# Kernel optimization log

Hardware: AMD Instinct MI355X
Metric: run time of the kernel (lower is better)

The kernel has to match this reference:

```python
import jax, jax.numpy as jnp
import numpy as np

B, S, D, H = 2, 2048, 1024, 16
DH = D // H  # 64

def setup_inputs() -> dict:
    key = jax.random.key(0)
    ks = jax.random.split(key, 11)
    sc = 1.0 / np.sqrt(D)
    return {
        "query": jax.random.normal(ks[0], (B, S, D), jnp.float32),
        "key":   jax.random.normal(ks[1], (B, S, D), jnp.float32),
        "value": jax.random.normal(ks[2], (B, S, D), jnp.float32),
        "Wq": jax.random.normal(ks[3], (D, D), jnp.float32) * sc,
        "bq": jnp.zeros((D,), jnp.float32),
        "Wk": jax.random.normal(ks[4], (D, D), jnp.float32) * sc,
        "bk": jnp.zeros((D,), jnp.float32),
        "Wv": jax.random.normal(ks[5], (D, D), jnp.float32) * sc,
        "bv": jnp.zeros((D,), jnp.float32),
        "Wo": jax.random.normal(ks[6], (D, D), jnp.float32) * sc,
        "bo": jnp.zeros((D,), jnp.float32),
    }

def reference(query, key, value, Wq, bq, Wk, bk, Wv, bv, Wo, bo):
    # torch Linear: y = x @ W^T + b
    def split_heads(x):  # (B,S,D) -> (B,H,S,DH)
        return x.reshape(B, S, H, DH).transpose(0, 2, 1, 3)
    Q = split_heads(query @ Wq.T + bq)
    K = split_heads(key   @ Wk.T + bk)
    V = split_heads(value @ Wv.T + bv)
    scores = jnp.einsum('bhqd,bhkd->bhqk', Q, K) / jnp.sqrt(jnp.float32(DH))
    # Original applies torch.softmax(scores, dim=1) on a (B*H, Sq, Sk) tensor,
    # i.e. normalization over the QUERY axis -> axis=-2 here (faithful to source).
    attn = jax.nn.softmax(scores, axis=-2)
    # dropout omitted for deterministic reference (identity / eval mode)
    out = jnp.einsum('bhqk,bhkd->bhqd', attn, V)  # (B,H,S,DH)
    out = out.transpose(0, 2, 1, 3).reshape(B, S, D)
    return out @ Wo.T + bo
```

## Files before the change

### kernel.cpp

```cpp
#include <hip/hip_runtime.h>
#include <hip/hip_bf16.h>
#include <math.h>

#define BB 2
#define SS 2048
#define DD 1024
#define HH 16
#define DH 64

typedef __bf16 bf16;
typedef __bf16 bf16x8 __attribute__((ext_vector_type(8)));
typedef __bf16 bf16x4 __attribute__((ext_vector_type(4)));
typedef short short4v __attribute__((ext_vector_type(4)));
typedef float f32x4 __attribute__((ext_vector_type(4)));

static const size_t NTOK  = (size_t)BB * SS * DD;


__device__ __forceinline__ f32x4 mfma16(bf16x8 a, bf16x8 b, f32x4 c) {
    return __builtin_amdgcn_mfma_f32_16x16x32_bf16(a, b, c, 0, 0, 0);
}
__device__ __forceinline__ f32x4 mfma16k16(short4v a, short4v b, f32x4 c) {
    return __builtin_amdgcn_mfma_f32_16x16x16bf16_1k(a, b, c, 0, 0, 0);
}
__device__ __forceinline__ void gload_lds16(const void* g, void* l) {
    __builtin_amdgcn_global_load_lds(
        (const __attribute__((address_space(1))) void*)g,
        (__attribute__((address_space(3))) void*)l, 16, 0, 0);
}
__device__ __forceinline__ bf16x8 cvt8(float4 a, float4 b) {
    bf16x8 r;
    r[0] = (bf16)a.x; r[1] = (bf16)a.y; r[2] = (bf16)a.z; r[3] = (bf16)a.w;
    r[4] = (bf16)b.x; r[5] = (bf16)b.y; r[6] = (bf16)b.z; r[7] = (bf16)b.w;
    return r;
}

#define WAITV(N)  asm volatile("s_waitcnt vmcnt(" #N ")" ::: "memory")
#define BAR()     __builtin_amdgcn_s_barrier()

__global__ void signal_f(float* out, float v) {
    if (threadIdx.x == 0 && blockIdx.x == 0) out[0] = v;
}

__global__ __launch_bounds__(256) void cvt_bf16(
    const float* __restrict__ s, bf16* __restrict__ d)
{
    size_t i = ((size_t)blockIdx.x * 256 + threadIdx.x) * 8;
    float4 a = *(const float4*)(s + i);
    float4 b = *(const float4*)(s + i + 4);
    *(bf16x8*)(d + i) = cvt8(a, b);
}
__global__ __launch_bounds__(256) void cvt_w3(
    const float* __restrict__ w0, const float* __restrict__ w1,
    const float* __restrict__ w2, bf16* __restrict__ o0,
    bf16* __restrict__ o1, bf16* __restrict__ o2)
{
    const float* s = (blockIdx.y == 0) ? w0 : (blockIdx.y == 1) ? w1 : w2;
    bf16*        d = (blockIdx.y == 0) ? o0 : (blockIdx.y == 1) ? o1 : o2;
    size_t i = ((size_t)blockIdx.x * 256 + threadIdx.x) * 8;
    float4 a = *(const float4*)(s + i);
    float4 b = *(const float4*)(s + i + 4);
    *(bf16x8*)(d + i) = cvt8(a, b);
}

#define LDP3 40

__global__ __launch_bounds__(256, 3) void qkv4(
    const float* __restrict__ Aq, const float* __restrict__ Ak,
    const float* __restrict__ Av,
    const bf16* __restrict__ Wqb, const bf16* __restrict__ Wkb,
    const bf16* __restrict__ Wvb,
    const float* __restrict__ bq, const float* __restrict__ bk,
    const float* __restrict__ bv,
    bf16* __restrict__ Qs, bf16* __restrict__ Ks, bf16* __restrict__ Vt)
{
    const int K = DD, N = DD;
    __shared__ bf16 As[2][128][LDP3];
    __shared__ bf16 Bs[2][128][LDP3];

    int t = (int)threadIdx.x;
    int lane = t & 63, w = t >> 6;
    int wm = w >> 1, wn = w & 1;
    int c16 = lane & 15, quad = lane >> 4, ko = quad << 3;

    int x = blockIdx.x & 7;
    int j = blockIdx.x >> 3;
    int proj = j >> 5;
    int rem  = j & 31;
    int tm = x + ((rem >> 3) << 3);
    int tn = rem & 7;

    const float* A    = (proj == 0) ? Aq : (proj == 1) ? Ak : Av;
    const bf16*  W    = (proj == 0) ? Wqb : (proj == 1) ? Wkb : Wvb;
    const float* bias = (proj == 0) ? bq : (proj == 1) ? bk : bv;
    bf16*        C    = (proj == 0) ? Qs : (proj == 1) ? Ks : Vt;
    float osc = (proj == 0) ? 0.125f : 1.0f;

    int arow = t >> 1, acb = (t & 1) * 16;
    const float* abase = A + (size_t)(tm * 128 + arow) * K + acb;
    const bf16*  wbase = W + (size_t)(tn * 128 + arow) * K + acb;

    f32x4 acc[4][4];
#pragma unroll
    for (int i = 0; i < 4; ++i)
#pragma unroll
        for (int q = 0; q < 4; ++q) acc[i][q] = (f32x4){0.f, 0.f, 0.f, 0.f};

    float4 av0, av1, av2, av3;
    bf16x8 wv0, wv1;
    av0 = *(const float4*)(abase);     av1 = *(const float4*)(abase + 4);
    av2 = *(const float4*)(abase + 8); av3 = *(const float4*)(abase + 12);
    wv0 = *(const bf16x8*)(wbase);
    wv1 = *(const bf16x8*)(wbase + 8);
    *(bf16x8*)&As[0][arow][acb]     = cvt8(av0, av1);
    *(bf16x8*)&As[0][arow][acb + 8] = cvt8(av2, av3);
    *(bf16x8*)&Bs[0][arow][acb]     = wv0;
    *(bf16x8*)&Bs[0][arow][acb + 8] = wv1;
    __syncthreads();

    int bi = 0;
    for (int k0 = 0; k0 < K; k0 += 32) {
        int kn = k0 + 32;
        if (kn < K) {
            av0 = *(const float4*)(abase + kn);
            av1 = *(const float4*)(abase + kn + 4);
            av2 = *(const float4*)(abase + kn + 8);
            av3 = *(const float4*)(abase + kn + 12);
            wv0 = *(const bf16x8*)(wbase + kn);
            wv1 = *(const bf16x8*)(wbase + kn + 8);
        }
        bf16x8 af[4], bfr[4];
#pragma unroll
        for (int mt = 0; mt < 4; ++mt)
            af[mt] = *(const bf16x8*)&As[bi][wm * 64 + mt * 16 + c16][ko];
#pragma unroll
        for (int nt = 0; nt < 4; ++nt)
            bfr[nt] = *(const bf16x8*)&Bs[bi][wn * 64 + nt * 16 + c16][ko];
#pragma unroll
        for (int mt = 0; mt < 4; ++mt)
#pragma unroll
            for (int nt = 0; nt < 4; ++nt)
                acc[mt][nt] = mfma16(af[mt], bfr[nt], acc[mt][nt]);

        if (kn < K) {
            *(bf16x8*)&As[bi ^ 1][arow][acb]     = cvt8(av0, av1);
            *(bf16x8*)&As[bi ^ 1][arow][acb + 8] = cvt8(av2, av3);
            *(bf16x8*)&Bs[bi ^ 1][arow][acb]     = wv0;
            *(bf16x8*)&Bs[bi ^ 1][arow][acb + 8] = wv1;
        }
        __syncthreads();
        bi ^= 1;
    }

#pragma unroll
    for (int nt = 0; nt < 4; ++nt) {
        int col = tn * 128 + wn * 64 + nt * 16 + c16;
        float bv2 = bias[col];
#pragma unroll
        for (int mt = 0; mt < 4; ++mt) {
            int r0 = tm * 128 + wm * 64 + mt * 16 + quad * 4;
            if (proj == 2) {
                int b2 = r0 >> 11;
                int s  = r0 & (SS - 1);
                size_t base = ((size_t)b2 * N + col) * SS + s;
                bf16x4 pk;
#pragma unroll
                for (int r = 0; r < 4; ++r)
                    pk[r] = (bf16)(acc[mt][nt][r] + bv2);
                *(bf16x4*)&C[base] = pk;
            } else {
#pragma unroll
                for (int r = 0; r < 4; ++r)
                    C[(size_t)(r0 + r) * N + col] =
                        (bf16)((acc[mt][nt][r] + bv2) * osc);
            }
        }
    }
}

__global__ __launch_bounds__(256) void gemm5(
    const bf16* __restrict__ A, const bf16* __restrict__ W,
    const float* __restrict__ bias, float* __restrict__ C)
{
    __shared__ __align__(16) bf16 As[4][128][32];
    __shared__ __align__(16) bf16 Bs[4][128][32];

    int t = (int)threadIdx.x;
    int lane = t & 63, w = t >> 6;
    int wm = w >> 1, wn = w & 1;
    int c16 = lane & 15, quad = lane >> 4, ko = quad << 3;

    int x = blockIdx.x & 7, j = blockIdx.x >> 3;
    int tm = x + ((j >> 3) << 3);
    int tn = j & 7;

    int wr0 = lane >> 2;
    int wsw = (lane & 3) ^ (wr0 & 3);
    const bf16* asrc = A + (size_t)(tm * 128 + w * 32 + wr0) * DD + wsw * 8;
    const bf16* wsrc = W + (size_t)(tn * 128 + w * 32 + wr0) * DD + wsw * 8;
    char* adst = (char*)&As[0][0][0] + w * 2048;
    char* wdst = (char*)&Bs[0][0][0] + w * 2048;

    f32x4 acc[4][4];
#pragma unroll
    for (int i = 0; i < 4; ++i)
#pragma unroll
        for (int q = 0; q < 4; ++q) acc[i][q] = (f32x4){0.f, 0.f, 0.f, 0.f};

#pragma unroll
    for (int s = 0; s < 2; ++s) {
        gload_lds16(asrc + s * 32, adst + s * 8192);
        gload_lds16(asrc + (size_t)16 * DD + s * 32, adst + s * 8192 + 1024);
        gload_lds16(wsrc + s * 32, wdst + s * 8192);
        gload_lds16(wsrc + (size_t)16 * DD + s * 32, wdst + s * 8192 + 1024);
    }

    for (int t0 = 0; t0 < 32; ++t0) {
        if (t0 + 2 < 32) {
            int s = t0 + 2, sb = (s & 3) * 8192;
            gload_lds16(asrc + s * 32, adst + sb);
            gload_lds16(asrc + (size_t)16 * DD + s * 32, adst + sb + 1024);
            gload_lds16(wsrc + s * 32, wdst + sb);
            gload_lds16(wsrc + (size_t)16 * DD + s * 32, wdst + sb + 1024);
        }
        if (t0 < 30)      { WAITV(8); }
        else if (t0 == 30){ WAITV(4); }
        else              { WAITV(0); }
        BAR();
        const char* al = (const char*)&As[0][0][0] + (t0 & 3) * 8192;
        const char* wl = (const char*)&Bs[0][0][0] + (t0 & 3) * 8192;
        bf16x8 af[4], bfr[4];
#pragma unroll
        for (int mt = 0; mt < 4; ++mt) {
            int row = wm * 64 + mt * 16 + c16;
            af[mt] = *(const bf16x8*)(al + row * 64 + ((quad ^ (row & 3)) << 4));
        }
#pragma unroll
        for (int nt = 0; nt < 4; ++nt) {
            int row = wn * 64 + nt * 16 + c16;
            bfr[nt] = *(const bf16x8*)(wl + row * 64 + ((quad ^ (row & 3)) << 4));
        }
#pragma unroll
        for (int mt = 0; mt < 4; ++mt)
#pragma unroll
            for (int nt = 0; nt < 4; ++nt)
                acc[mt][nt] = mfma16(af[mt], bfr[nt], acc[mt][nt]);
    }

#pragma unroll
    for (int nt = 0; nt < 4; ++nt) {
        int col = tn * 128 + wn * 64 + nt * 16 + c16;
        float bv = bias[col];
#pragma unroll
        for (int mt = 0; mt < 4; ++mt) {
            int r0 = tm * 128 + wm * 64 + mt * 16 + quad * 4;
#pragma unroll
            for (int r = 0; r < 4; ++r)
                C[(size_t)(r0 + r) * DD + col] = acc[mt][nt][r] + bv;
        }
    }
}

__global__ __launch_bounds__(512) void col_stats4(
    const bf16* __restrict__ Q, const bf16* __restrict__ Km,
    float* __restrict__ rzS)
{
    __shared__ __align__(16) bf16 Qlds[4][32][64];

    int t = (int)threadIdx.x;
    int w = t >> 6, lane = t & 63;
    int c16 = lane & 15, quad = lane >> 4, ko = quad << 3;

    int x = blockIdx.x & 7, j = blockIdx.x >> 3;
    int bh = ((j >> 3) << 3) + x;
    int kg = j & 7;
    int b = bh >> 4, h = bh & (HH - 1);
    int kbase = kg * 256 + w * 32;

    bf16x8 kf[2][2];
#pragma unroll
    for (int g = 0; g < 2; ++g) {
        const bf16* kp =
            Km + ((size_t)(b * SS + kbase + g * 16 + c16)) * DD + h * DH + ko;
        kf[g][0] = *(const bf16x8*)kp;
        kf[g][1] = *(const bf16x8*)(kp + 32);
    }

    int srow  = ((w & 3) << 3) + (lane >> 3);
    int schnk = (lane & 7) ^ (srow & 7);
    const bf16* gsrc = Q + ((size_t)(b * SS + srow)) * DD + h * DH + schnk * 8;
    int ldsOff = (w & 3) << 10;
    bool stager = (w < 4);

    float z[2][4] = {{0.f,0.f,0.f,0.f},{0.f,0.f,0.f,0.f}};

    if (stager) {
        gload_lds16(gsrc, (char*)&Qlds[0][0][0] + ldsOff);
        gload_lds16(gsrc + (size_t)32 * DD, (char*)&Qlds[1][0][0] + ldsOff);
    }

    for (int t0 = 0; t0 < 64; ++t0) {
        if (t0 + 2 < 64 && stager)
            gload_lds16(gsrc + (size_t)(t0 + 2) * 32 * DD,
                        (char*)&Qlds[(t0 + 2) & 3][0][0] + ldsOff);
        if (t0 < 62)      { WAITV(2); }
        else if (t0 == 62){ WAITV(1); }
        else              { WAITV(0); }
        BAR();
        const char* ql = (const char*)&Qlds[t0 & 3][0][0];
#pragma unroll
        for (int qs = 0; qs < 2; ++qs) {
            int row = qs * 16 + c16;
            int p0  = quad ^ (row & 7);
            bf16x8 qf0 = *(const bf16x8*)(ql + row * 128 + p0 * 16);
            bf16x8 qf1 = *(const bf16x8*)(ql + row * 128 + (p0 ^ 4) * 16);
#pragma unroll
            for (int g = 0; g < 2; ++g) {
                f32x4 a = {0.f, 0.f, 0.f, 0.f};
                a = mfma16(kf[g][0], qf0, a);
                a = mfma16(kf[g][1], qf1, a);
#pragma unroll
                for (int r = 0; r < 4; ++r)
                    z[g][r] += __expf(a[r]);
            }
        }
    }

#pragma unroll
    for (int g = 0; g < 2; ++g)
#pragma unroll
        for (int r = 0; r < 4; ++r) {
#pragma unroll
            for (int off = 1; off < 16; off <<= 1)
                z[g][r] += __shfl_xor(z[g][r], off, 64);
        }
    if (c16 == 0) {
        size_t base = (size_t)bh * SS + kbase + quad * 4;
#pragma unroll
        for (int g = 0; g < 2; ++g)
#pragma unroll
            for (int r = 0; r < 4; ++r)
                rzS[base + g * 16 + r] = 1.0f / z[g][r];
    }
}

__global__ __launch_bounds__(512) void attn_ctx6(
    const bf16* __restrict__ Q, const bf16* __restrict__ Km,
    const bf16* __restrict__ Vt, const float* __restrict__ rzS,
    bf16* __restrict__ ctx)
{
    __shared__ __align__(16) char lds[4][8192];

    int t = (int)threadIdx.x;
    int w = t >> 6, lane = t & 63;
    int c16 = lane & 15, quad = lane >> 4, ko = quad << 3;

    int bid = blockIdx.x;
    int x = bid & 7, j = bid >> 3;
    int bh = ((j >> 3) << 3) + x;
    int qg = j & 7;
    int b = bh >> 4, h = bh & (HH - 1);
    int qt0 = qg * 16 + w * 2;

    const bf16* qp0 = Q + ((size_t)(b * SS + qt0 * 16 + c16)) * DD + h * DH + ko;
    bf16x8 qa0 = *(const bf16x8*)qp0;
    bf16x8 qa1 = *(const bf16x8*)(qp0 + 32);
    const bf16* qp1 = qp0 + (size_t)16 * DD;
    bf16x8 qb0 = *(const bf16x8*)qp1;
    bf16x8 qb1 = *(const bf16x8*)(qp1 + 32);

    const bf16* gsrc;
    int ldsOff;
    bool isK = (w < 4);
    if (isK) {
        int row   = (w << 3) + (lane >> 3);
        int chunk = (lane & 7) ^ (row & 7);
        gsrc  = Km + ((size_t)(b * SS + row)) * DD + h * DH + chunk * 8;
        ldsOff = (w << 10);
    } else {
        int i = w - 4;
        int row   = (i << 4) + (lane >> 2);
        int chunk = (lane & 3) ^ (row & 3);
        gsrc  = Vt + ((size_t)(b * DD + h * DH + row)) * SS + chunk * 8;
        ldsOff = 4096 + (i << 10);
    }

    int kread  = c16 * 128 + ((quad ^ (c16 & 7)) << 4);
    int vread0 = c16 * 64 + (((quad >> 1) ^ (c16 & 3)) << 4) + ((quad & 1) << 3);

    const float* rzp = rzS + (size_t)bh * SS + quad * 4;

    f32x4 oa[4] = {{0,0,0,0},{0,0,0,0},{0,0,0,0},{0,0,0,0}};
    f32x4 ob[4] = {{0,0,0,0},{0,0,0,0},{0,0,0,0},{0,0,0,0}};

    gload_lds16(gsrc, &lds[0][ldsOff]);
    gload_lds16(isK ? gsrc + (size_t)32 * DD : gsrc + 32, &lds[1][ldsOff]);

    for (int t0 = 0; t0 < 64; ++t0) {
        if (t0 + 2 < 64) {
            int s = t0 + 2;
            const bf16* g = isK ? gsrc + (size_t)(s * 32) * DD : gsrc + s * 32;
            gload_lds16(g, &lds[s & 3][ldsOff]);
        }
        if (t0 < 62)      { WAITV(2); }
        else if (t0 == 62){ WAITV(1); }
        else              { WAITV(0); }
        BAR();
        const char* kl = &lds[t0 & 3][0];
        const char* vl = &lds[t0 & 3][4096];
        int kb = t0 * 32;
#pragma unroll
        for (int ks = 0; ks < 2; ++ks) {
            int kb0 = kread + ks * 2048;
            bf16x8 kf0 = *(const bf16x8*)(kl + kb0);
            bf16x8 kf1 = *(const bf16x8*)(kl + (kb0 ^ 64));
            f32x4 z4 = *(const f32x4*)(rzp + kb + ks * 16);
            f32x4 sa = {0,0,0,0}, sb = {0,0,0,0};
            sa = mfma16(kf0, qa0, sa);
            sa = mfma16(kf1, qa1, sa);
            sb = mfma16(kf0, qb0, sb);
            sb = mfma16(kf1, qb1, sb);

            union { bf16x4 b; short4v s; } pa, pb;
#pragma unroll
            for (int r = 0; r < 4; ++r) {
                pa.b[r] = (bf16)(__expf(sa[r]) * z4[r]);
                pb.b[r] = (bf16)(__expf(sb[r]) * z4[r]);
            }
            int vb0 = ks ? (vread0 ^ 32) : vread0;
#pragma unroll
            for (int dt = 0; dt < 4; ++dt) {
                short4v vf = *(const short4v*)(vl + vb0 + dt * 1024);
                oa[dt] = mfma16k16(pa.s, vf, oa[dt]);
                ob[dt] = mfma16k16(pb.s, vf, ob[dt]);
            }
        }
    }

    size_t orow = ((size_t)(b * SS + qt0 * 16 + quad * 4)) * DD + h * DH + c16;
#pragma unroll
    for (int dt = 0; dt < 4; ++dt)
#pragma unroll
        for (int r = 0; r < 4; ++r) {
            ctx[orow + (size_t)r * DD + dt * 16] = (bf16)oa[dt][r];
            ctx[orow + (size_t)(16 + r) * DD + dt * 16] = (bf16)ob[dt][r];
        }
}

extern "C" void kernel_launch(void* const* d_in, const int* in_sizes, int n_in,
                              void* d_out, int out_size, void* d_ws, size_t ws_size,
                              hipStream_t stream) {
    const float* query = (const float*)d_in[0];
    const float* key   = (const float*)d_in[1];
    const float* value = (const float*)d_in[2];
    const float* Wq = (const float*)d_in[3];
    const float* bq = (const float*)d_in[4];
    const float* Wk = (const float*)d_in[5];
    const float* bk = (const float*)d_in[6];
    const float* Wv = (const float*)d_in[7];
    const float* bv = (const float*)d_in[8];
    const float* Wo = (const float*)d_in[9];
    const float* bo = (const float*)d_in[10];
    float* out = (float*)d_out;

    if (n_in != 11 || in_sizes[0] != (int)NTOK || in_sizes[3] != DD * DD ||
        in_sizes[4] != DD || out_size != (int)NTOK) {
        hipLaunchKernelGGL(signal_f, dim3(1), dim3(64), 0, stream, out, -64.0f);
        return;
    }

    bf16* Qs  = (bf16*)d_ws;
    bf16* Ks  = Qs + NTOK;
    bf16* Vt  = Ks + NTOK;
    bf16* Cs  = Vt + NTOK;
    float* rzS = (float*)(Cs + NTOK);

    bf16* Wqb = Cs;
    bf16* Wkb = Cs + (size_t)DD * DD;
    bf16* Wvb = Cs + (size_t)2 * DD * DD;
    bf16* WoB = Qs;

    hipLaunchKernelGGL(cvt_w3, dim3(512, 3), dim3(256), 0, stream,
                       Wq, Wk, Wv, Wqb, Wkb, Wvb);

    hipLaunchKernelGGL(qkv4, dim3(768), dim3(256), 0, stream,
                       query, key, value, Wqb, Wkb, Wvb, bq, bk, bv,
                       Qs, Ks, Vt);

    hipLaunchKernelGGL(col_stats4, dim3(256), dim3(512), 0, stream, Qs, Ks, rzS);

    hipLaunchKernelGGL(attn_ctx6, dim3(256), dim3(512), 0, stream,
                       Qs, Ks, Vt, rzS, Cs);

    hipLaunchKernelGGL(cvt_bf16, dim3(512), dim3(256), 0, stream, Wo, WoB);

    hipLaunchKernelGGL(gemm5, dim3(256), dim3(256), 0, stream, Cs, WoB, bo, out);
}
```

Measured before the change: 288.8 us.

## Split column stats over query halves, deepen QKV prefetch, widen output GEMM blocks

```diff
diff --git a/kernel.cpp b/kernel.cpp
--- a/kernel.cpp
+++ b/kernel.cpp
@@ -15,6 +15,7 @@
 typedef float f32x4 __attribute__((ext_vector_type(4)));
 
 static const size_t NTOK  = (size_t)BB * SS * DD;
+static const size_t STATN = (size_t)BB * HH * SS;
 
 
 __device__ __forceinline__ f32x4 mfma16(bf16x8 a, bf16x8 b, f32x4 c) {
@@ -65,7 +66,7 @@
 
 #define LDP3 40
 
-__global__ __launch_bounds__(256, 3) void qkv4(
+__global__ __launch_bounds__(256, 3) void qkv6(
     const float* __restrict__ Aq, const float* __restrict__ Ak,
     const float* __restrict__ Av,
     const bf16* __restrict__ Wqb, const bf16* __restrict__ Wkb,
@@ -106,50 +107,59 @@
 #pragma unroll
         for (int q = 0; q < 4; ++q) acc[i][q] = (f32x4){0.f, 0.f, 0.f, 0.f};
 
-    float4 av0, av1, av2, av3;
-    bf16x8 wv0, wv1;
-    av0 = *(const float4*)(abase);     av1 = *(const float4*)(abase + 4);
-    av2 = *(const float4*)(abase + 8); av3 = *(const float4*)(abase + 12);
-    wv0 = *(const bf16x8*)(wbase);
-    wv1 = *(const bf16x8*)(wbase + 8);
-    *(bf16x8*)&As[0][arow][acb]     = cvt8(av0, av1);
-    *(bf16x8*)&As[0][arow][acb + 8] = cvt8(av2, av3);
-    *(bf16x8*)&Bs[0][arow][acb]     = wv0;
-    *(bf16x8*)&Bs[0][arow][acb + 8] = wv1;
+    float4 aA0, aA1, aA2, aA3, aB0, aB1, aB2, aB3;
+    bf16x8 wA0, wA1, wB0, wB1;
+
+    aA0 = *(const float4*)(abase);     aA1 = *(const float4*)(abase + 4);
+    aA2 = *(const float4*)(abase + 8); aA3 = *(const float4*)(abase + 12);
+    wA0 = *(const bf16x8*)(wbase);     wA1 = *(const bf16x8*)(wbase + 8);
+    *(bf16x8*)&As[0][arow][acb]     = cvt8(aA0, aA1);
+    *(bf16x8*)&As[0][arow][acb + 8] = cvt8(aA2, aA3);
+    *(bf16x8*)&Bs[0][arow][acb]     = wA0;
+    *(bf16x8*)&Bs[0][arow][acb + 8] = wA1;
+    aB0 = *(const float4*)(abase + 32);     aB1 = *(const float4*)(abase + 36);
+    aB2 = *(const float4*)(abase + 40);     aB3 = *(const float4*)(abase + 44);
+    wB0 = *(const bf16x8*)(wbase + 32);     wB1 = *(const bf16x8*)(wbase + 40);
     __syncthreads();
 
-    int bi = 0;
-    for (int k0 = 0; k0 < K; k0 += 32) {
-        int kn = k0 + 32;
-        if (kn < K) {
-            av0 = *(const float4*)(abase + kn);
-            av1 = *(const float4*)(abase + kn + 4);
-            av2 = *(const float4*)(abase + kn + 8);
-            av3 = *(const float4*)(abase + kn + 12);
-            wv0 = *(const bf16x8*)(wbase + kn);
-            wv1 = *(const bf16x8*)(wbase + kn + 8);
+    auto qstep = [&](int T0, int BI,
+                     float4& cA0, float4& cA1, float4& cA2, float4& cA3,
+                     bf16x8& cW0, bf16x8& cW1,
+                     float4& nA0, float4& nA1, float4& nA2, float4& nA3,
+                     bf16x8& nW0, bf16x8& nW1) {
+        if (T0 + 2 < 32) {
+            const float* ap = abase + (T0 + 2) * 32;
+            nA0 = *(const float4*)(ap);     nA1 = *(const float4*)(ap + 4);
+            nA2 = *(const float4*)(ap + 8); nA3 = *(const float4*)(ap + 12);
+            const bf16* wp = wbase + (T0 + 2) * 32;
+            nW0 = *(const bf16x8*)(wp);     nW1 = *(const bf16x8*)(wp + 8);
         }
         bf16x8 af[4], bfr[4];
 #pragma unroll
         for (int mt = 0; mt < 4; ++mt)
-            af[mt] = *(const bf16x8*)&As[bi][wm * 64 + mt * 16 + c16][ko];
+            af[mt] = *(const bf16x8*)&As[BI][wm * 64 + mt * 16 + c16][ko];
 #pragma unroll
         for (int nt = 0; nt < 4; ++nt)
-            bfr[nt] = *(const bf16x8*)&Bs[bi][wn * 64 + nt * 16 + c16][ko];
+            bfr[nt] = *(const bf16x8*)&Bs[BI][wn * 64 + nt * 16 + c16][ko];
 #pragma unroll
         for (int mt = 0; mt < 4; ++mt)
 #pragma unroll
             for (int nt = 0; nt < 4; ++nt)
                 acc[mt][nt] = mfma16(af[mt], bfr[nt], acc[mt][nt]);
-
-        if (kn < K) {
-            *(bf16x8*)&As[bi ^ 1][arow][acb]     = cvt8(av0, av1);
-            *(bf16x8*)&As[bi ^ 1][arow][acb + 8] = cvt8(av2, av3);
-            *(bf16x8*)&Bs[bi ^ 1][arow][acb]     = wv0;
-            *(bf16x8*)&Bs[bi ^ 1][arow][acb + 8] = wv1;
+        if (T0 + 1 < 32) {
+            *(bf16x8*)&As[BI ^ 1][arow][acb]     = cvt8(cA0, cA1);
+            *(bf16x8*)&As[BI ^ 1][arow][acb + 8] = cvt8(cA2, cA3);
+            *(bf16x8*)&Bs[BI ^ 1][arow][acb]     = cW0;
+            *(bf16x8*)&Bs[BI ^ 1][arow][acb + 8] = cW1;
         }
         __syncthreads();
-        bi ^= 1;
+    };
+
+    for (int i = 0; i < 16; ++i) {
+        qstep(2 * i,     0, aB0, aB1, aB2, aB3, wB0, wB1,
+                            aA0, aA1, aA2, aA3, wA0, wA1);
+        qstep(2 * i + 1, 1, aA0, aA1, aA2, aA3, wA0, wA1,
+                            aB0, aB1, aB2, aB3, wB0, wB1);
     }
 
 #pragma unroll
@@ -178,7 +188,7 @@
     }
 }
 
-__global__ __launch_bounds__(256) void gemm5(
+__global__ __launch_bounds__(512) void gemm6(
     const bf16* __restrict__ A, const bf16* __restrict__ W,
     const float* __restrict__ bias, float* __restrict__ C)
 {
@@ -187,69 +197,65 @@
 
     int t = (int)threadIdx.x;
     int lane = t & 63, w = t >> 6;
-    int wm = w >> 1, wn = w & 1;
+    int wm = w >> 2, wn = w & 3;
     int c16 = lane & 15, quad = lane >> 4, ko = quad << 3;
 
     int x = blockIdx.x & 7, j = blockIdx.x >> 3;
     int tm = x + ((j >> 3) << 3);
     int tn = j & 7;
 
-    int wr0 = lane >> 2;
-    int wsw = (lane & 3) ^ (wr0 & 3);
-    const bf16* asrc = A + (size_t)(tm * 128 + w * 32 + wr0) * DD + wsw * 8;
-    const bf16* wsrc = W + (size_t)(tn * 128 + w * 32 + wr0) * DD + wsw * 8;
-    char* adst = (char*)&As[0][0][0] + w * 2048;
-    char* wdst = (char*)&Bs[0][0][0] + w * 2048;
-
-    f32x4 acc[4][4];
+    int row0 = w * 16 + (lane >> 2);
+    int chnk = (lane & 3) ^ (row0 & 3);
+    const bf16* asrc = A + (size_t)(tm * 128 + row0) * DD + chnk * 8;
+    const bf16* wsrc = W + (size_t)(tn * 128 + row0) * DD + chnk * 8;
+    char* adst = (char*)&As[0][0][0] + w * 1024;
+    char* wdst = (char*)&Bs[0][0][0] + w * 1024;
+
+    f32x4 acc[4][2];
 #pragma unroll
     for (int i = 0; i < 4; ++i)
 #pragma unroll
-        for (int q = 0; q < 4; ++q) acc[i][q] = (f32x4){0.f, 0.f, 0.f, 0.f};
+        for (int q = 0; q < 2; ++q) acc[i][q] = (f32x4){0.f, 0.f, 0.f, 0.f};
 
 #pragma unroll
     for (int s = 0; s < 2; ++s) {
         gload_lds16(asrc + s * 32, adst + s * 8192);
-        gload_lds16(asrc + (size_t)16 * DD + s * 32, adst + s * 8192 + 1024);
         gload_lds16(wsrc + s * 32, wdst + s * 8192);
-        gload_lds16(wsrc + (size_t)16 * DD + s * 32, wdst + s * 8192 + 1024);
     }
 
     for (int t0 = 0; t0 < 32; ++t0) {
         if (t0 + 2 < 32) {
             int s = t0 + 2, sb = (s & 3) * 8192;
             gload_lds16(asrc + s * 32, adst + sb);
-            gload_lds16(asrc + (size_t)16 * DD + s * 32, adst + sb + 1024);
             gload_lds16(wsrc + s * 32, wdst + sb);
-            gload_lds16(wsrc + (size_t)16 * DD + s * 32, wdst + sb + 1024);
-        }
-        if (t0 < 30)      { WAITV(8); }
-        else if (t0 == 30){ WAITV(4); }
+        }
+        if (t0 < 30)      { WAITV(4); }
+        else if (t0 == 30){ WAITV(2); }
         else              { WAITV(0); }
         BAR();
         const char* al = (const char*)&As[0][0][0] + (t0 & 3) * 8192;
         const char* wl = (const char*)&Bs[0][0][0] + (t0 & 3) * 8192;
-        bf16x8 af[4], bfr[4];
+        bf16x8 af[4], bfr[2];
 #pragma unroll
         for (int mt = 0; mt < 4; ++mt) {
             int row = wm * 64 + mt * 16 + c16;
             af[mt] = *(const bf16x8*)(al + row * 64 + ((quad ^ (row & 3)) << 4));
         }
 #pragma unroll
-        for (int nt = 0; nt < 4; ++nt) {
-            int row = wn * 64 + nt * 16 + c16;
+        for (int nt = 0; nt < 2; ++nt) {
+            int row = wn * 32 + nt * 16 + c16;
             bfr[nt] = *(const bf16x8*)(wl + row * 64 + ((quad ^ (row & 3)) << 4));
         }
 #pragma unroll
         for (int mt = 0; mt < 4; ++mt)
 #pragma unroll
-            for (int nt = 0; nt < 4; ++nt)
+            for (int nt = 0; nt < 2; ++nt)
                 acc[mt][nt] = mfma16(af[mt], bfr[nt], acc[mt][nt]);
     }
 
 #pragma unroll
-    for (int nt = 0; nt < 4; ++nt) {
-        int col = tn * 128 + wn * 64 + nt * 16 + c16;
+    for (int nt = 0; nt < 2; ++nt) {
+        int col = tn * 128 + wn * 32 + nt * 16 + c16;
         float bv = bias[col];
 #pragma unroll
         for (int mt = 0; mt < 4; ++mt) {
@@ -261,9 +267,9 @@
     }
 }
 
-__global__ __launch_bounds__(512) void col_stats4(
+__global__ __launch_bounds__(512) void col_stats5(
     const bf16* __restrict__ Q, const bf16* __restrict__ Km,
-    float* __restrict__ rzS)
+    float* __restrict__ z0S, float* __restrict__ z1S)
 {
     __shared__ __align__(16) bf16 Qlds[4][32][64];
 
@@ -272,10 +278,13 @@
     int c16 = lane & 15, quad = lane >> 4, ko = quad << 3;
 
     int x = blockIdx.x & 7, j = blockIdx.x >> 3;
-    int bh = ((j >> 3) << 3) + x;
+    int bh = ((j >> 4) << 3) + x;
+    int qh = (j >> 3) & 1;
     int kg = j & 7;
     int b = bh >> 4, h = bh & (HH - 1);
     int kbase = kg * 256 + w * 32;
+    int q0base = qh * 1024;
+    float* zS = qh ? z1S : z0S;
 
     bf16x8 kf[2][2];
 #pragma unroll
@@ -288,7 +297,8 @@
 
     int srow  = ((w & 3) << 3) + (lane >> 3);
     int schnk = (lane & 7) ^ (srow & 7);
-    const bf16* gsrc = Q + ((size_t)(b * SS + srow)) * DD + h * DH + schnk * 8;
+    const bf16* gsrc =
+        Q + ((size_t)(b * SS + q0base + srow)) * DD + h * DH + schnk * 8;
     int ldsOff = (w & 3) << 10;
     bool stager = (w < 4);
 
@@ -299,12 +309,12 @@
         gload_lds16(gsrc + (size_t)32 * DD, (char*)&Qlds[1][0][0] + ldsOff);
     }
 
-    for (int t0 = 0; t0 < 64; ++t0) {
-        if (t0 + 2 < 64 && stager)
+    for (int t0 = 0; t0 < 32; ++t0) {
+        if (t0 + 2 < 32 && stager)
             gload_lds16(gsrc + (size_t)(t0 + 2) * 32 * DD,
                         (char*)&Qlds[(t0 + 2) & 3][0][0] + ldsOff);
-        if (t0 < 62)      { WAITV(2); }
-        else if (t0 == 62){ WAITV(1); }
+        if (t0 < 30)      { WAITV(2); }
+        else if (t0 == 30){ WAITV(1); }
         else              { WAITV(0); }
         BAR();
         const char* ql = (const char*)&Qlds[t0 & 3][0][0];
@@ -340,16 +350,17 @@
         for (int g = 0; g < 2; ++g)
 #pragma unroll
             for (int r = 0; r < 4; ++r)
-                rzS[base + g * 16 + r] = 1.0f / z[g][r];
-    }
-}
-
-__global__ __launch_bounds__(512) void attn_ctx6(
+                zS[base + g * 16 + r] = z[g][r];
+    }
+}
+
+__global__ __launch_bounds__(512) void attn_ctx7(
     const bf16* __restrict__ Q, const bf16* __restrict__ Km,
-    const bf16* __restrict__ Vt, const float* __restrict__ rzS,
-    bf16* __restrict__ ctx)
+    const bf16* __restrict__ Vt, const float* __restrict__ z0S,
+    const float* __restrict__ z1S, bf16* __restrict__ ctx)
 {
     __shared__ __align__(16) char lds[4][8192];
+    __shared__ __align__(16) float rzlds[2048];
 
     int t = (int)threadIdx.x;
     int w = t >> 6, lane = t & 63;
@@ -368,6 +379,22 @@
     const bf16* qp1 = qp0 + (size_t)16 * DD;
     bf16x8 qb0 = *(const bf16x8*)qp1;
     bf16x8 qb1 = *(const bf16x8*)(qp1 + 32);
+
+    {
+        const float* z0p = z0S + (size_t)bh * SS + (w << 8) + lane * 4;
+        const float* z1p = z1S + (size_t)bh * SS + (w << 8) + lane * 4;
+        gload_lds16(z0p, (char*)&lds[0][0] + (w << 10));
+        gload_lds16(z1p, (char*)&lds[1][0] + (w << 10));
+        WAITV(0);
+        __syncthreads();
+        f32x4 z0 = *(const f32x4*)&lds[0][t * 16];
+        f32x4 z1 = *(const f32x4*)&lds[1][t * 16];
+        f32x4 rz;
+#pragma unroll
+        for (int r = 0; r < 4; ++r) rz[r] = 1.0f / (z0[r] + z1[r]);
+        *(f32x4*)&rzlds[t * 4] = rz;
+        __syncthreads();
+    }
 
     const bf16* gsrc;
     int ldsOff;
@@ -380,15 +407,14 @@
     } else {
         int i = w - 4;
         int row   = (i << 4) + (lane >> 2);
-        int chunk = (lane & 3) ^ (row & 3);
+        int chunk = (lane & 3) ^ ((lane >> 3) & 3);
         gsrc  = Vt + ((size_t)(b * DD + h * DH + row)) * SS + chunk * 8;
         ldsOff = 4096 + (i << 10);
     }
 
     int kread  = c16 * 128 + ((quad ^ (c16 & 7)) << 4);
-    int vread0 = c16 * 64 + (((quad >> 1) ^ (c16 & 3)) << 4) + ((quad & 1) << 3);
-
-    const float* rzp = rzS + (size_t)bh * SS + quad * 4;
+    int vread0 = c16 * 64 + (((quad >> 1) ^ ((c16 >> 1) & 3)) << 4)
+               + ((quad & 1) << 3);
 
     f32x4 oa[4] = {{0,0,0,0},{0,0,0,0},{0,0,0,0},{0,0,0,0}};
     f32x4 ob[4] = {{0,0,0,0},{0,0,0,0},{0,0,0,0},{0,0,0,0}};
@@ -408,13 +434,12 @@
         BAR();
         const char* kl = &lds[t0 & 3][0];
         const char* vl = &lds[t0 & 3][4096];
-        int kb = t0 * 32;
 #pragma unroll
         for (int ks = 0; ks < 2; ++ks) {
             int kb0 = kread + ks * 2048;
             bf16x8 kf0 = *(const bf16x8*)(kl + kb0);
             bf16x8 kf1 = *(const bf16x8*)(kl + (kb0 ^ 64));
-            f32x4 z4 = *(const f32x4*)(rzp + kb + ks * 16);
+            f32x4 z4 = *(const f32x4*)&rzlds[t0 * 32 + ks * 16 + quad * 4];
             f32x4 sa = {0,0,0,0}, sb = {0,0,0,0};
             sa = mfma16(kf0, qa0, sa);
             sa = mfma16(kf1, qa1, sa);
@@ -473,7 +498,8 @@
     bf16* Ks  = Qs + NTOK;
     bf16* Vt  = Ks + NTOK;
     bf16* Cs  = Vt + NTOK;
-    float* rzS = (float*)(Cs + NTOK);
+    float* z0S = (float*)(Cs + NTOK);
+    float* z1S = z0S + STATN;
 
     bf16* Wqb = Cs;
     bf16* Wkb = Cs + (size_t)DD * DD;
@@ -483,16 +509,17 @@
     hipLaunchKernelGGL(cvt_w3, dim3(512, 3), dim3(256), 0, stream,
                        Wq, Wk, Wv, Wqb, Wkb, Wvb);
 
-    hipLaunchKernelGGL(qkv4, dim3(768), dim3(256), 0, stream,
+    hipLaunchKernelGGL(qkv6, dim3(768), dim3(256), 0, stream,
                        query, key, value, Wqb, Wkb, Wvb, bq, bk, bv,
                        Qs, Ks, Vt);
 
-    hipLaunchKernelGGL(col_stats4, dim3(256), dim3(512), 0, stream, Qs, Ks, rzS);
-
-    hipLaunchKernelGGL(attn_ctx6, dim3(256), dim3(512), 0, stream,
-                       Qs, Ks, Vt, rzS, Cs);
+    hipLaunchKernelGGL(col_stats5, dim3(512), dim3(512), 0, stream,
+                       Qs, Ks, z0S, z1S);
+
+    hipLaunchKernelGGL(attn_ctx7, dim3(256), dim3(512), 0, stream,
+                       Qs, Ks, Vt, z0S, z1S, Cs);
 
     hipLaunchKernelGGL(cvt_bf16, dim3(512), dim3(256), 0, stream, Wo, WoB);
 
-    hipLaunchKernelGGL(gemm5, dim3(256), dim3(256), 0, stream, Cs, WoB, bo, out);
-}
+    hipLaunchKernelGGL(gemm6, dim3(256), dim3(512), 0, stream, Cs, WoB, bo, out);
+}
```

New measurement: 271.5 us. -6.0%, faster.
